# Performance work log

Hardware: AMD Instinct MI355X
Metric: run time of the kernel (lower is better)

Reference implementation:

```python
import jax, jax.numpy as jnp
import numpy as np

NEG_SLOPE = 0.2  # PyG GATConv default negative_slope


def _gat_conv(x, src, dst, W, a_src, a_dst, bias, heads, concat):
    """PyG-style GATConv (eval mode, self-loops already appended to src/dst).
    x: [N, Fin], W: [Fin, heads*C], a_src/a_dst: [heads, C], bias matches output.
    """
    N = x.shape[0]
    C = W.shape[1] // heads
    xw = (x @ W).reshape(N, heads, C)                      # [N, H, C]
    alpha_s = jnp.sum(xw * a_src, axis=-1)                 # [N, H]
    alpha_d = jnp.sum(xw * a_dst, axis=-1)                 # [N, H]
    e = jax.nn.leaky_relu(alpha_s[src] + alpha_d[dst], NEG_SLOPE)  # [E, H]
    # softmax over incoming edges of each destination node (numerically stable)
    m = jax.ops.segment_max(e, dst, num_segments=N)        # [N, H]
    e = jnp.exp(e - m[dst])
    denom = jax.ops.segment_sum(e, dst, num_segments=N)    # [N, H]
    alpha = e / denom[dst]                                 # [E, H]
    out = jax.ops.segment_sum(alpha[:, :, None] * xw[src], dst, num_segments=N)  # [N, H, C]
    if concat:
        out = out.reshape(N, heads * C)
    else:
        out = out.mean(axis=1)
    return out + bias


def setup_inputs() -> dict:
    key = jax.random.key(0)
    ks = jax.random.split(key, 10)
    N, E, FIN, FOUT, H1, C1 = 100000, 1600000, 128, 16, 4, 8
    x = jax.random.normal(ks[0], (N, FIN), jnp.float32)
    edge_index = jax.random.randint(ks[1], (2, E), 0, N, dtype=jnp.int32)
    W1 = jax.random.normal(ks[2], (FIN, H1 * C1), jnp.float32) / np.sqrt(FIN)
    a1_src = jax.random.normal(ks[3], (H1, C1), jnp.float32) / np.sqrt(C1)
    a1_dst = jax.random.normal(ks[4], (H1, C1), jnp.float32) / np.sqrt(C1)
    b1 = jnp.zeros((H1 * C1,), jnp.float32)
    W2 = jax.random.normal(ks[5], (H1 * C1, FOUT), jnp.float32) / np.sqrt(H1 * C1)
    a2_src = jax.random.normal(ks[6], (1, FOUT), jnp.float32) / np.sqrt(FOUT)
    a2_dst = jax.random.normal(ks[7], (1, FOUT), jnp.float32) / np.sqrt(FOUT)
    b2 = jnp.zeros((FOUT,), jnp.float32)
    return {"x": x, "edge_index": edge_index, "W1": W1, "a1_src": a1_src,
            "a1_dst": a1_dst, "b1": b1, "W2": W2, "a2_src": a2_src,
            "a2_dst": a2_dst, "b2": b2}


def reference(x, edge_index, W1, a1_src, a1_dst, b1, W2, a2_src, a2_dst, b2):
    N = x.shape[0]
    # PyG GATConv add_self_loops=True default
    loop = jnp.arange(N, dtype=edge_index.dtype)
    src = jnp.concatenate([edge_index[0], loop])
    dst = jnp.concatenate([edge_index[1], loop])
    # eval mode: F.dropout is identity
    h = _gat_conv(x, src, dst, W1, a1_src, a1_dst, b1, heads=4, concat=True)
    h = jax.nn.elu(h)
    h = _gat_conv(h, src, dst, W2, a2_src, a2_dst, b2, heads=1, concat=True)
    return jax.nn.log_softmax(h, axis=1)
```

## Files before the change

kernel.cpp:

```cpp
#include <hip/hip_runtime.h>
#include <math.h>

#define NN 100000
#define NE 1600000
#define ET (NE + NN)
#define FIN 128
#define H1 4
#define C1 8
#define F1 32
#define FOUT 16
#define NSLOPE 0.2f

#define PARTW 256
#define PSHIFT 8
#define NPART ((NN + PARTW - 1) / PARTW)
#define CHUNK 8192
#define NBLK ((ET + CHUNK - 1) / CHUNK)
#define CPAD 16
#define SMASK 0x1FFFF

typedef _Float16 half8 __attribute__((ext_vector_type(8)));
typedef _Float16 half4_t __attribute__((ext_vector_type(4)));
typedef _Float16 half2_t __attribute__((ext_vector_type(2)));
typedef float f32x4 __attribute__((ext_vector_type(4)));

template <int SEL>
__device__ inline float fp8dec(unsigned int w) {
    return __builtin_amdgcn_cvt_f32_fp8((int)w, SEL);
}


__device__ inline int wave_incl_scan(int v) {
#pragma unroll
    for (int off = 1; off < 64; off <<= 1) {
        int u = __shfl_up(v, off);
        if ((threadIdx.x & 63) >= off) v += u;
    }
    return v;
}

__device__ inline int block_excl_scan(int v, int* wsum, int nw) {
    int t = threadIdx.x, wid = t >> 6, lane = t & 63;
    int incl = wave_incl_scan(v);
    if (lane == 63) wsum[wid] = incl;
    __syncthreads();
    if (wid == 0) {
        int wv = (lane < nw) ? wsum[lane] : 0;
        wv = wave_incl_scan(wv);
        if (lane < nw) wsum[lane] = wv;
    }
    __syncthreads();
    return incl - v + (wid ? wsum[wid - 1] : 0);
}


__global__ __launch_bounds__(1024) void k_hist(const int* __restrict__ dstA, int* __restrict__ ptotal) {
    __shared__ int h[NPART];
    int t = threadIdx.x;
    for (int i = t; i < NPART; i += 1024) h[i] = 0;
    __syncthreads();
    int base = blockIdx.x * CHUNK;
#pragma unroll
    for (int k = 0; k < CHUNK / 1024; k++) {
        int e = base + k * 1024 + t;
        if (e < ET) {
            int d = (e < NE) ? dstA[e] : (e - NE);
            atomicAdd(&h[d >> PSHIFT], 1);
        }
    }
    __syncthreads();
    for (int i = t; i < NPART; i += 1024)
        if (h[i]) atomicAdd(&ptotal[i * CPAD], h[i]);
}

__global__ __launch_bounds__(512) void k_pbase(const int* __restrict__ ptotal, int* __restrict__ pbase,
                                               int* __restrict__ gcur, int* __restrict__ rowstart) {
    __shared__ int wsum[8];
    int t = threadIdx.x;
    int v = (t < NPART) ? ptotal[t * CPAD] : 0;
    int excl = block_excl_scan(v, wsum, 8);
    if (t < NPART) { pbase[t] = excl; gcur[t * CPAD] = excl; }
    if (t == 0) { pbase[NPART] = ET; rowstart[NN] = ET; }
}

__global__ __launch_bounds__(1024) void k_part(const int* __restrict__ srcA, const int* __restrict__ dstA,
                                               int* __restrict__ gcur, int* __restrict__ pairs) {
    __shared__ int h[NPART];
    __shared__ int cur[NPART];
    int t = threadIdx.x;
    for (int i = t; i < NPART; i += 1024) h[i] = 0;
    __syncthreads();
    int base = blockIdx.x * CHUNK;
#pragma unroll
    for (int k = 0; k < CHUNK / 1024; k++) {
        int e = base + k * 1024 + t;
        if (e < ET) {
            int d = (e < NE) ? dstA[e] : (e - NE);
            atomicAdd(&h[d >> PSHIFT], 1);
        }
    }
    __syncthreads();
    for (int i = t; i < NPART; i += 1024) {
        int c = h[i];
        cur[i] = c ? atomicAdd(&gcur[i * CPAD], c) : 0;
    }
    __syncthreads();
#pragma unroll
    for (int k = 0; k < CHUNK / 1024; k++) {
        int e = base + k * 1024 + t;
        if (e < ET) {
            int s, d;
            if (e < NE) { s = srcA[e]; d = dstA[e]; }
            else        { s = e - NE;  d = s; }
            int pos = atomicAdd(&cur[d >> PSHIFT], 1);
            pairs[pos] = ((d & (PARTW - 1)) << 17) | s;
        }
    }
}

__global__ __launch_bounds__(1024) void k_sort(const int* __restrict__ pbase, const int* __restrict__ pairs,
                                               int* __restrict__ rowstart, int* __restrict__ epack) {
    __shared__ int hist[PARTW];
    __shared__ int sa[PARTW], sb[PARTW];
    int p = blockIdx.x;
    int t = threadIdx.x;
    int n0 = p << PSHIFT;
    int nn = min(PARTW, NN - n0);
    int base = pbase[p];
    int cnt = pbase[p + 1] - base;
    if (t < PARTW) hist[t] = 0;
    __syncthreads();
    for (int i = t; i < cnt; i += 1024)
        atomicAdd(&hist[pairs[base + i] >> 17], 1);
    __syncthreads();
    if (t < PARTW) sa[t] = hist[t];
    __syncthreads();
    int* pin = sa; int* pout = sb;
    for (int off = 1; off < PARTW; off <<= 1) {
        if (t < PARTW) pout[t] = pin[t] + ((t >= off) ? pin[t - off] : 0);
        __syncthreads();
        int* tmp = pin; pin = pout; pout = tmp;
    }
    int excl = 0;
    if (t < PARTW) {
        excl = pin[t] - hist[t];
        if (t < nn) rowstart[n0 + t] = base + excl;
    }
    __syncthreads();
    if (t < PARTW) hist[t] = excl;
    __syncthreads();
    for (int i = t; i < cnt; i += 1024) {
        int v = pairs[base + i];
        int pos = base + atomicAdd(&hist[v >> 17], 1);
        epack[pos] = v;
    }
}


__global__ __launch_bounds__(256) void k_gemm1(const float* __restrict__ x, const float* __restrict__ W1,
        const float* __restrict__ a1s, const float* __restrict__ a1d,
        unsigned int* __restrict__ xc1, float* __restrict__ ad1) {
    __shared__ _Float16 w1t[F1 * FIN];
    __shared__ float xs[256 * F1];
    int t = threadIdx.x;
    {
        int i0 = t * 16;
#pragma unroll
        for (int i = 0; i < 16; i++) {
            int idx = i0 + i;
            int k = idx >> 5, n = idx & 31;
            w1t[n * FIN + k] = (_Float16)W1[idx];
        }
    }
    __syncthreads();
    int w = t >> 6, l = t & 63;
    int q = l >> 4, r16 = l & 15;
    int nblk = blockIdx.x * 256;
    int n0 = nblk + w * 64;
    half8 bf[4][2];
#pragma unroll
    for (int kc = 0; kc < 4; kc++)
#pragma unroll
        for (int nt = 0; nt < 2; nt++)
            bf[kc][nt] = *(const half8*)&w1t[(nt * 16 + r16) * FIN + kc * 32 + q * 8];
#pragma unroll
    for (int mt = 0; mt < 4; mt++) {
        int row = n0 + mt * 16 + r16;
        int rowc = min(row, NN - 1);
        const float4* xp = (const float4*)(x + (size_t)rowc * FIN + q * 8);
        half8 af[4];
#pragma unroll
        for (int kc = 0; kc < 4; kc++) {
            float4 u = xp[kc * 8];
            float4 v = xp[kc * 8 + 1];
            half8 a;
            a[0] = (_Float16)u.x; a[1] = (_Float16)u.y; a[2] = (_Float16)u.z; a[3] = (_Float16)u.w;
            a[4] = (_Float16)v.x; a[5] = (_Float16)v.y; a[6] = (_Float16)v.z; a[7] = (_Float16)v.w;
            af[kc] = a;
        }
        f32x4 acc0 = {0.f, 0.f, 0.f, 0.f};
        f32x4 acc1 = {0.f, 0.f, 0.f, 0.f};
#pragma unroll
        for (int kc = 0; kc < 4; kc++) {
            acc0 = __builtin_amdgcn_mfma_f32_16x16x32_f16(af[kc], bf[kc][0], acc0, 0, 0, 0);
            acc1 = __builtin_amdgcn_mfma_f32_16x16x32_f16(af[kc], bf[kc][1], acc1, 0, 0, 0);
        }
#pragma unroll
        for (int r = 0; r < 4; r++) {
            xs[(w * 64 + mt * 16 + q * 4 + r) * F1 + r16] = acc0[r];
            xs[(w * 64 + mt * 16 + q * 4 + r) * F1 + 16 + r16] = acc1[r];
        }
    }
    int node = nblk + w * 64 + l;
    if (node < NN) {
        const float4* xr = (const float4*)&xs[(w * 64 + l) * F1];
        float rowv[F1];
#pragma unroll
        for (int j = 0; j < 8; j++) {
            float4 v = xr[j];
            rowv[j * 4] = v.x; rowv[j * 4 + 1] = v.y; rowv[j * 4 + 2] = v.z; rowv[j * 4 + 3] = v.w;
        }
        uint4 o[3];
        unsigned int* ow = (unsigned int*)o;
#pragma unroll
        for (int c4 = 0; c4 < 8; c4++) {
            int p = 0;
            p = __builtin_amdgcn_cvt_pk_fp8_f32(rowv[c4 * 4 + 0], rowv[c4 * 4 + 1], p, false);
            p = __builtin_amdgcn_cvt_pk_fp8_f32(rowv[c4 * 4 + 2], rowv[c4 * 4 + 3], p, true);
            ow[c4] = (unsigned int)p;
        }
        float ss[H1], dd[H1];
#pragma unroll
        for (int h = 0; h < H1; h++) {
            ss[h] = 0.f; dd[h] = 0.f;
#pragma unroll
            for (int c = 0; c < C1; c++) {
                ss[h] = fmaf(rowv[h * C1 + c], a1s[h * C1 + c], ss[h]);
                dd[h] = fmaf(rowv[h * C1 + c], a1d[h * C1 + c], dd[h]);
            }
        }
#pragma unroll
        for (int h = 0; h < H1; h++) ow[8 + h] = __float_as_uint(ss[h]);
        uint4* o16 = (uint4*)(xc1 + (size_t)node * 16);
        o16[0] = o[0];
        o16[1] = o[1];
        o16[2] = o[2];
        ((float4*)ad1)[node] = make_float4(dd[0], dd[1], dd[2], dd[3]);
    }
}


__global__ __launch_bounds__(256) void k_gather1(const int* __restrict__ rowstart, const int* __restrict__ epack,
        const float* __restrict__ ad1, const unsigned int* __restrict__ xc1,
        const float* __restrict__ b1, _Float16* __restrict__ h1h) {
    int n = blockIdx.x * 4 + (threadIdx.x >> 6);
    if (n >= NN) return;
    int l = threadIdx.x & 63;
    int g = l >> 3;
    int j = l & 7;
    int h = j >> 1;
    float adh = ad1[n * H1 + h];
    int beg = rowstart[n], end = rowstart[n + 1];
    int endm1 = end - 1;
    float a0 = 0.f, a1 = 0.f, a2 = 0.f, a3 = 0.f, ad = 0.f;
    int i = beg + g;
    int i0 = min(i, endm1), i1 = min(i + 8, endm1);
    int c0 = epack[i0] & SMASK, c1 = epack[i1] & SMASK;
    int i2 = min(i + 16, endm1), i3 = min(i + 24, endm1);
    int sn0 = epack[i2] & SMASK, sn1 = epack[i3] & SMASK;
    float f0 = __uint_as_float(xc1[c0 * 16 + 8 + h]);
    float f1 = __uint_as_float(xc1[c1 * 16 + 8 + h]);
    unsigned int v0 = xc1[c0 * 16 + j], v1 = xc1[c1 * 16 + j];
    while (i + 8 < end) {
        float nf0 = __uint_as_float(xc1[sn0 * 16 + 8 + h]);
        float nf1 = __uint_as_float(xc1[sn1 * 16 + 8 + h]);
        unsigned int nv0 = xc1[sn0 * 16 + j], nv1 = xc1[sn1 * 16 + j];
        int p0 = min(i + 32, endm1), p1 = min(i + 40, endm1);
        int u0 = epack[p0] & SMASK, u1 = epack[p1] & SMASK;
        float e0 = f0 + adh, e1 = f1 + adh;
        e0 = (e0 > 0.f) ? e0 : NSLOPE * e0;
        e1 = (e1 > 0.f) ? e1 : NSLOPE * e1;
        float w0 = __expf(e0), w1 = __expf(e1);
        ad += w0 + w1;
        a0 = fmaf(w0, fp8dec<0>(v0), fmaf(w1, fp8dec<0>(v1), a0));
        a1 = fmaf(w0, fp8dec<1>(v0), fmaf(w1, fp8dec<1>(v1), a1));
        a2 = fmaf(w0, fp8dec<2>(v0), fmaf(w1, fp8dec<2>(v1), a2));
        a3 = fmaf(w0, fp8dec<3>(v0), fmaf(w1, fp8dec<3>(v1), a3));
        f0 = nf0; f1 = nf1; v0 = nv0; v1 = nv1;
        sn0 = u0; sn1 = u1;
        i += 16;
    }
    if (i < end) {
        float e0 = f0 + adh;
        e0 = (e0 > 0.f) ? e0 : NSLOPE * e0;
        float w0 = __expf(e0);
        ad += w0;
        a0 = fmaf(w0, fp8dec<0>(v0), a0);
        a1 = fmaf(w0, fp8dec<1>(v0), a1);
        a2 = fmaf(w0, fp8dec<2>(v0), a2);
        a3 = fmaf(w0, fp8dec<3>(v0), a3);
    }
#pragma unroll
    for (int off = 8; off < 64; off <<= 1) {
        a0 += __shfl_xor(a0, off);
        a1 += __shfl_xor(a1, off);
        a2 += __shfl_xor(a2, off);
        a3 += __shfl_xor(a3, off);
        ad += __shfl_xor(ad, off);
    }
    if (l < 8) {
        float inv = 1.0f / ad;
        float y0 = fmaf(a0, inv, b1[4 * j]);
        float y1 = fmaf(a1, inv, b1[4 * j + 1]);
        float y2 = fmaf(a2, inv, b1[4 * j + 2]);
        float y3 = fmaf(a3, inv, b1[4 * j + 3]);
        y0 = (y0 > 0.f) ? y0 : expm1f(y0);
        y1 = (y1 > 0.f) ? y1 : expm1f(y1);
        y2 = (y2 > 0.f) ? y2 : expm1f(y2);
        y3 = (y3 > 0.f) ? y3 : expm1f(y3);
        half4_t o;
        o[0] = (_Float16)y0; o[1] = (_Float16)y1; o[2] = (_Float16)y2; o[3] = (_Float16)y3;
        ((half4_t*)h1h)[(size_t)n * 8 + j] = o;
    }
}


__global__ __launch_bounds__(256) void k_node2(const _Float16* __restrict__ h1h, const float* __restrict__ W2,
        const float* __restrict__ a2s, const float* __restrict__ a2d,
        unsigned int* __restrict__ xc2, float* __restrict__ ad2) {
    int n = blockIdx.x * 256 + threadIdx.x;
    if (n >= NN) return;
    float acc[FOUT];
#pragma unroll
    for (int j = 0; j < FOUT; j++) acc[j] = 0.f;
    const half8* h8 = (const half8*)(h1h + (size_t)n * F1);
#pragma unroll
    for (int i8 = 0; i8 < F1 / 8; i8++) {
        half8 hv = h8[i8];
#pragma unroll
        for (int kk = 0; kk < 8; kk++) {
            float hk = (float)hv[kk];
            int i = i8 * 8 + kk;
#pragma unroll
            for (int j = 0; j < FOUT; j++)
                acc[j] = fmaf(hk, W2[i * FOUT + j], acc[j]);
        }
    }
    float ss = 0.f, dd = 0.f;
#pragma unroll
    for (int j = 0; j < FOUT; j++) {
        ss = fmaf(acc[j], a2s[j], ss);
        dd = fmaf(acc[j], a2d[j], dd);
    }
    uint4 o[2];
    unsigned int* ow = (unsigned int*)o;
#pragma unroll
    for (int p = 0; p < 8; p++) {
        half2_t hp;
        hp[0] = (_Float16)acc[2 * p];
        hp[1] = (_Float16)acc[2 * p + 1];
        ow[p] = *(unsigned int*)&hp;
    }
    uint4* o16 = (uint4*)(xc2 + (size_t)n * 16);
    o16[0] = o[0];
    o16[1] = o[1];
    xc2[(size_t)n * 16 + 8] = __float_as_uint(ss);
    ad2[n] = dd;
}


__global__ __launch_bounds__(256) void k_gather2(const int* __restrict__ rowstart, const int* __restrict__ epack,
        const float* __restrict__ ad2, const unsigned int* __restrict__ xc2,
        const float* __restrict__ b2, float* __restrict__ out) {
    int n = blockIdx.x * 4 + (threadIdx.x >> 6);
    if (n >= NN) return;
    int l = threadIdx.x & 63;
    int g = l >> 3;
    int j = l & 7;
    float adn = ad2[n];
    const half2_t* xw = (const half2_t*)xc2;
    int beg = rowstart[n], end = rowstart[n + 1];
    int endm1 = end - 1;
    float a0 = 0.f, a1v = 0.f, ad = 0.f;
    int i = beg + g;
    int i0 = min(i, endm1), i1 = min(i + 8, endm1);
    int c0 = epack[i0] & SMASK, c1 = epack[i1] & SMASK;
    int i2 = min(i + 16, endm1), i3 = min(i + 24, endm1);
    int sn0 = epack[i2] & SMASK, sn1 = epack[i3] & SMASK;
    float f0 = __uint_as_float(xc2[c0 * 16 + 8]);
    float f1 = __uint_as_float(xc2[c1 * 16 + 8]);
    half2_t v0 = xw[c0 * 16 + j], v1 = xw[c1 * 16 + j];
    while (i + 8 < end) {
        float nf0 = __uint_as_float(xc2[sn0 * 16 + 8]);
        float nf1 = __uint_as_float(xc2[sn1 * 16 + 8]);
        half2_t nv0 = xw[sn0 * 16 + j], nv1 = xw[sn1 * 16 + j];
        int p0 = min(i + 32, endm1), p1 = min(i + 40, endm1);
        int u0 = epack[p0] & SMASK, u1 = epack[p1] & SMASK;
        float e0 = f0 + adn, e1 = f1 + adn;
        e0 = (e0 > 0.f) ? e0 : NSLOPE * e0;
        e1 = (e1 > 0.f) ? e1 : NSLOPE * e1;
        float w0 = __expf(e0), w1 = __expf(e1);
        ad += w0 + w1;
        a0  = fmaf(w0, (float)v0[0], fmaf(w1, (float)v1[0], a0));
        a1v = fmaf(w0, (float)v0[1], fmaf(w1, (float)v1[1], a1v));
        f0 = nf0; f1 = nf1; v0 = nv0; v1 = nv1;
        sn0 = u0; sn1 = u1;
        i += 16;
    }
    if (i < end) {
        float e0 = f0 + adn;
        e0 = (e0 > 0.f) ? e0 : NSLOPE * e0;
        float w0 = __expf(e0);
        ad += w0;
        a0  = fmaf(w0, (float)v0[0], a0);
        a1v = fmaf(w0, (float)v0[1], a1v);
    }
#pragma unroll
    for (int off = 8; off < 64; off <<= 1) {
        a0  += __shfl_xor(a0, off);
        a1v += __shfl_xor(a1v, off);
        ad  += __shfl_xor(ad, off);
    }
    float inv = 1.0f / ad;
    float y0 = fmaf(a0, inv, b2[2 * j]);
    float y1 = fmaf(a1v, inv, b2[2 * j + 1]);
    float m = fmaxf(y0, y1);
#pragma unroll
    for (int off = 1; off < 8; off <<= 1) m = fmaxf(m, __shfl_xor(m, off));
    float s = __expf(y0 - m) + __expf(y1 - m);
#pragma unroll
    for (int off = 1; off < 8; off <<= 1) s += __shfl_xor(s, off);
    float ls = logf(s);
    if (l < 8)
        ((float2*)out)[(size_t)n * 8 + j] = make_float2(y0 - m - ls, y1 - m - ls);
}


extern "C" void kernel_launch(void* const* d_in, const int* in_sizes, int n_in,
                              void* d_out, int out_size, void* d_ws, size_t ws_size,
                              hipStream_t stream) {
    const float* x   = (const float*)d_in[0];
    const int*   ei  = (const int*)d_in[1];
    const float* W1  = (const float*)d_in[2];
    const float* a1s = (const float*)d_in[3];
    const float* a1d = (const float*)d_in[4];
    const float* b1  = (const float*)d_in[5];
    const float* W2  = (const float*)d_in[6];
    const float* a2s = (const float*)d_in[7];
    const float* a2d = (const float*)d_in[8];
    const float* b2  = (const float*)d_in[9];
    float* out = (float*)d_out;

    const int* srcA = ei;
    const int* dstA = ei + NE;

    char* w = (char*)d_ws;
    size_t off = 0;
    auto carve = [&](size_t bytes) -> void* {
        void* p = w + off;
        off = (off + bytes + 255) & ~(size_t)255;
        return p;
    };
    size_t xc1_off = off;
    unsigned int* xc1 = (unsigned int*)carve((size_t)NN * 64);
    float* ad1     = (float*)carve((size_t)NN * H1 * 4);
    _Float16* h1h  = (_Float16*)carve((size_t)NN * F1 * 2);
    unsigned int* xc2 = (unsigned int*)carve((size_t)NN * 64);
    float* ad2     = (float*)carve((size_t)NN * 4);
    int* pairs     = (int*)(w + xc1_off);
    int* rowstart  = (int*)carve((size_t)(NN + 1) * 4);
    int* epack     = (int*)carve((size_t)(ET + 64) * 4);
    int* ptotal    = (int*)carve((size_t)NPART * CPAD * 4);
    int* gcur      = (int*)carve((size_t)NPART * CPAD * 4);
    int* pbase     = (int*)carve((size_t)(NPART + 1) * 4);
    (void)ws_size; (void)in_sizes; (void)n_in; (void)out_size;

    hipMemsetAsync(ptotal, 0, (size_t)NPART * CPAD * 4, stream);

    k_hist  <<<NBLK, 1024, 0, stream>>>(dstA, ptotal);
    k_pbase <<<1, 512, 0, stream>>>(ptotal, pbase, gcur, rowstart);
    k_part  <<<NBLK, 1024, 0, stream>>>(srcA, dstA, gcur, pairs);
    k_sort  <<<NPART, 1024, 0, stream>>>(pbase, pairs, rowstart, epack);

    k_gemm1 <<<(NN + 255) / 256, 256, 0, stream>>>(x, W1, a1s, a1d, xc1, ad1);
    k_gather1<<<(NN + 3) / 4, 256, 0, stream>>>(rowstart, epack, ad1, xc1, b1, h1h);
    k_node2 <<<(NN + 255) / 256, 256, 0, stream>>>(h1h, W2, a2s, a2d, xc2, ad2);
    k_gather2<<<(NN + 3) / 4, 256, 0, stream>>>(rowstart, epack, ad2, xc2, b2, out);
}
```

Baseline: 238.8 us.

## Interleave attention scores with features so each gather fetches one 8-byte load

The node feature rows (xc1, xc2) are re-laid out so each lane's packed feature word sits next to a copy of the matching source attention score. The gather kernels can then fetch both with one uint2 load instead of two separate 4-byte loads. The min() clamps on edge indices are dropped, so prefetches may read past a row's end into padding. LeakyReLU becomes fmaxf. The trade-off is a 64-byte row instead of 48 bytes for layer 1, plus duplicated score values and a reliance on padding for the unclamped prefetch reads.

```diff
diff --git a/kernel.cpp b/kernel.cpp
--- a/kernel.cpp
+++ b/kernel.cpp
@@ -220,31 +220,31 @@
             float4 v = xr[j];
             rowv[j * 4] = v.x; rowv[j * 4 + 1] = v.y; rowv[j * 4 + 2] = v.z; rowv[j * 4 + 3] = v.w;
         }
-        uint4 o[3];
+        float ss[H1], dd[H1];
+#pragma unroll
+        for (int h = 0; h < H1; h++) {
+            ss[h] = 0.f; dd[h] = 0.f;
+#pragma unroll
+            for (int c = 0; c < C1; c++) {
+                ss[h] = fmaf(rowv[h * C1 + c], a1s[h * C1 + c], ss[h]);
+                dd[h] = fmaf(rowv[h * C1 + c], a1d[h * C1 + c], dd[h]);
+            }
+        }
+        uint4 o[4];
         unsigned int* ow = (unsigned int*)o;
 #pragma unroll
         for (int c4 = 0; c4 < 8; c4++) {
             int p = 0;
             p = __builtin_amdgcn_cvt_pk_fp8_f32(rowv[c4 * 4 + 0], rowv[c4 * 4 + 1], p, false);
             p = __builtin_amdgcn_cvt_pk_fp8_f32(rowv[c4 * 4 + 2], rowv[c4 * 4 + 3], p, true);
-            ow[c4] = (unsigned int)p;
-        }
-        float ss[H1], dd[H1];
-#pragma unroll
-        for (int h = 0; h < H1; h++) {
-            ss[h] = 0.f; dd[h] = 0.f;
-#pragma unroll
-            for (int c = 0; c < C1; c++) {
-                ss[h] = fmaf(rowv[h * C1 + c], a1s[h * C1 + c], ss[h]);
-                dd[h] = fmaf(rowv[h * C1 + c], a1d[h * C1 + c], dd[h]);
-            }
-        }
-#pragma unroll
-        for (int h = 0; h < H1; h++) ow[8 + h] = __float_as_uint(ss[h]);
+            ow[2 * c4] = (unsigned int)p;
+            ow[2 * c4 + 1] = __float_as_uint(ss[c4 >> 1]);
+        }
         uint4* o16 = (uint4*)(xc1 + (size_t)node * 16);
         o16[0] = o[0];
         o16[1] = o[1];
         o16[2] = o[2];
+        o16[3] = o[3];
         ((float4*)ad1)[node] = make_float4(dd[0], dd[1], dd[2], dd[3]);
     }
 }
@@ -260,39 +260,35 @@
     int j = l & 7;
     int h = j >> 1;
     float adh = ad1[n * H1 + h];
+    const uint2* xrow = (const uint2*)xc1;
     int beg = rowstart[n], end = rowstart[n + 1];
-    int endm1 = end - 1;
     float a0 = 0.f, a1 = 0.f, a2 = 0.f, a3 = 0.f, ad = 0.f;
     int i = beg + g;
-    int i0 = min(i, endm1), i1 = min(i + 8, endm1);
-    int c0 = epack[i0] & SMASK, c1 = epack[i1] & SMASK;
-    int i2 = min(i + 16, endm1), i3 = min(i + 24, endm1);
-    int sn0 = epack[i2] & SMASK, sn1 = epack[i3] & SMASK;
-    float f0 = __uint_as_float(xc1[c0 * 16 + 8 + h]);
-    float f1 = __uint_as_float(xc1[c1 * 16 + 8 + h]);
-    unsigned int v0 = xc1[c0 * 16 + j], v1 = xc1[c1 * 16 + j];
+    int c0 = epack[i] & SMASK, c1 = epack[i + 8] & SMASK;
+    int sn0 = epack[i + 16] & SMASK, sn1 = epack[i + 24] & SMASK;
+    uint2 t0 = xrow[c0 * 8 + j], t1 = xrow[c1 * 8 + j];
+    unsigned int v0 = t0.x, v1 = t1.x;
+    float f0 = __uint_as_float(t0.y), f1 = __uint_as_float(t1.y);
     while (i + 8 < end) {
-        float nf0 = __uint_as_float(xc1[sn0 * 16 + 8 + h]);
-        float nf1 = __uint_as_float(xc1[sn1 * 16 + 8 + h]);
-        unsigned int nv0 = xc1[sn0 * 16 + j], nv1 = xc1[sn1 * 16 + j];
-        int p0 = min(i + 32, endm1), p1 = min(i + 40, endm1);
-        int u0 = epack[p0] & SMASK, u1 = epack[p1] & SMASK;
+        uint2 n0v = xrow[sn0 * 8 + j], n1v = xrow[sn1 * 8 + j];
+        int u0 = epack[i + 32] & SMASK, u1 = epack[i + 40] & SMASK;
         float e0 = f0 + adh, e1 = f1 + adh;
-        e0 = (e0 > 0.f) ? e0 : NSLOPE * e0;
-        e1 = (e1 > 0.f) ? e1 : NSLOPE * e1;
+        e0 = fmaxf(e0, NSLOPE * e0);
+        e1 = fmaxf(e1, NSLOPE * e1);
         float w0 = __expf(e0), w1 = __expf(e1);
         ad += w0 + w1;
         a0 = fmaf(w0, fp8dec<0>(v0), fmaf(w1, fp8dec<0>(v1), a0));
         a1 = fmaf(w0, fp8dec<1>(v0), fmaf(w1, fp8dec<1>(v1), a1));
         a2 = fmaf(w0, fp8dec<2>(v0), fmaf(w1, fp8dec<2>(v1), a2));
         a3 = fmaf(w0, fp8dec<3>(v0), fmaf(w1, fp8dec<3>(v1), a3));
-        f0 = nf0; f1 = nf1; v0 = nv0; v1 = nv1;
+        v0 = n0v.x; v1 = n1v.x;
+        f0 = __uint_as_float(n0v.y); f1 = __uint_as_float(n1v.y);
         sn0 = u0; sn1 = u1;
         i += 16;
     }
     if (i < end) {
         float e0 = f0 + adh;
-        e0 = (e0 > 0.f) ? e0 : NSLOPE * e0;
+        e0 = fmaxf(e0, NSLOPE * e0);
         float w0 = __expf(e0);
         ad += w0;
         a0 = fmaf(w0, fp8dec<0>(v0), a0);
@@ -352,19 +348,22 @@
         ss = fmaf(acc[j], a2s[j], ss);
         dd = fmaf(acc[j], a2d[j], dd);
     }
-    uint4 o[2];
+    uint4 o[4];
     unsigned int* ow = (unsigned int*)o;
+    unsigned int ssu = __float_as_uint(ss);
 #pragma unroll
     for (int p = 0; p < 8; p++) {
         half2_t hp;
         hp[0] = (_Float16)acc[2 * p];
         hp[1] = (_Float16)acc[2 * p + 1];
-        ow[p] = *(unsigned int*)&hp;
+        ow[2 * p] = *(unsigned int*)&hp;
+        ow[2 * p + 1] = ssu;
     }
     uint4* o16 = (uint4*)(xc2 + (size_t)n * 16);
     o16[0] = o[0];
     o16[1] = o[1];
-    xc2[(size_t)n * 16 + 8] = __float_as_uint(ss);
+    o16[2] = o[2];
+    o16[3] = o[3];
     ad2[n] = dd;
 }
 
@@ -378,38 +377,33 @@
     int g = l >> 3;
     int j = l & 7;
     float adn = ad2[n];
-    const half2_t* xw = (const half2_t*)xc2;
+    const uint2* xrow = (const uint2*)xc2;
     int beg = rowstart[n], end = rowstart[n + 1];
-    int endm1 = end - 1;
     float a0 = 0.f, a1v = 0.f, ad = 0.f;
     int i = beg + g;
-    int i0 = min(i, endm1), i1 = min(i + 8, endm1);
-    int c0 = epack[i0] & SMASK, c1 = epack[i1] & SMASK;
-    int i2 = min(i + 16, endm1), i3 = min(i + 24, endm1);
-    int sn0 = epack[i2] & SMASK, sn1 = epack[i3] & SMASK;
-    float f0 = __uint_as_float(xc2[c0 * 16 + 8]);
-    float f1 = __uint_as_float(xc2[c1 * 16 + 8]);
-    half2_t v0 = xw[c0 * 16 + j], v1 = xw[c1 * 16 + j];
+    int c0 = epack[i] & SMASK, c1 = epack[i + 8] & SMASK;
+    int sn0 = epack[i + 16] & SMASK, sn1 = epack[i + 24] & SMASK;
+    uint2 t0 = xrow[c0 * 8 + j], t1 = xrow[c1 * 8 + j];
+    half2_t v0 = *(half2_t*)&t0.x, v1 = *(half2_t*)&t1.x;
+    float f0 = __uint_as_float(t0.y), f1 = __uint_as_float(t1.y);
     while (i + 8 < end) {
-        float nf0 = __uint_as_float(xc2[sn0 * 16 + 8]);
-        float nf1 = __uint_as_float(xc2[sn1 * 16 + 8]);
-        half2_t nv0 = xw[sn0 * 16 + j], nv1 = xw[sn1 * 16 + j];
-        int p0 = min(i + 32, endm1), p1 = min(i + 40, endm1);
-        int u0 = epack[p0] & SMASK, u1 = epack[p1] & SMASK;
+        uint2 n0v = xrow[sn0 * 8 + j], n1v = xrow[sn1 * 8 + j];
+        int u0 = epack[i + 32] & SMASK, u1 = epack[i + 40] & SMASK;
         float e0 = f0 + adn, e1 = f1 + adn;
-        e0 = (e0 > 0.f) ? e0 : NSLOPE * e0;
-        e1 = (e1 > 0.f) ? e1 : NSLOPE * e1;
+        e0 = fmaxf(e0, NSLOPE * e0);
+        e1 = fmaxf(e1, NSLOPE * e1);
         float w0 = __expf(e0), w1 = __expf(e1);
         ad += w0 + w1;
         a0  = fmaf(w0, (float)v0[0], fmaf(w1, (float)v1[0], a0));
         a1v = fmaf(w0, (float)v0[1], fmaf(w1, (float)v1[1], a1v));
-        f0 = nf0; f1 = nf1; v0 = nv0; v1 = nv1;
+        v0 = *(half2_t*)&n0v.x; v1 = *(half2_t*)&n1v.x;
+        f0 = __uint_as_float(n0v.y); f1 = __uint_as_float(n1v.y);
         sn0 = u0; sn1 = u1;
         i += 16;
     }
     if (i < end) {
         float e0 = f0 + adn;
-        e0 = (e0 > 0.f) ? e0 : NSLOPE * e0;
+        e0 = fmaxf(e0, NSLOPE * e0);
         float w0 = __expf(e0);
         ad += w0;
         a0  = fmaf(w0, (float)v0[0], a0);
@@ -473,6 +467,7 @@
     int* ptotal    = (int*)carve((size_t)NPART * CPAD * 4);
     int* gcur      = (int*)carve((size_t)NPART * CPAD * 4);
     int* pbase     = (int*)carve((size_t)(NPART + 1) * 4);
+    carve((size_t)2 * 1024 * 1024);
     (void)ws_size; (void)in_sizes; (void)n_in; (void)out_size;
 
     hipMemsetAsync(ptotal, 0, (size_t)NPART * CPAD * 4, stream);
```

Result: no change. 240.9 us (+0.9%).
